# Kernel tuning notes

Measured on AMD Instinct MI355X. Metric: run time of the kernel, lower is better.

Reference implementation:

```python
import jax, jax.numpy as jnp
import numpy as np

N_USERS, N_ITEMS, N_GENRES = 31360, 6807, 18
TOTAL = N_USERS + N_ITEMS + N_GENRES          # 38185
OFFSET = TOTAL - N_GENRES                      # 38167
D = 16                                         # embedding_dim
B = 524288                                     # batch
MLP_DIMS = [64, 32, 16]
IN_DIM = 3 * D                                 # field_num * embedding_dim


def setup_inputs() -> dict:
    key = jax.random.key(0)
    ks = jax.random.split(key, 14)
    user = jax.random.randint(ks[0], (B, 1), 0, N_USERS)
    item = N_USERS + jax.random.randint(ks[1], (B, 1), 0, N_ITEMS)
    x_onehot = jnp.concatenate([user, item], axis=1)            # [B,2] global ids
    multi_hot = jax.random.randint(ks[2], (B, N_GENRES), 0, 2)  # [B,18] 0/1 mask
    s = 0.05
    emb_table = s * jax.random.normal(ks[3], (TOTAL, D), jnp.float32)
    fc_table = s * jax.random.normal(ks[4], (TOTAL, 1), jnp.float32)
    W1 = s * jax.random.normal(ks[5], (IN_DIM, MLP_DIMS[0]), jnp.float32)
    b1 = jnp.zeros((MLP_DIMS[0],), jnp.float32)
    W2 = s * jax.random.normal(ks[6], (MLP_DIMS[0], MLP_DIMS[1]), jnp.float32)
    b2 = jnp.zeros((MLP_DIMS[1],), jnp.float32)
    W3 = s * jax.random.normal(ks[7], (MLP_DIMS[1], MLP_DIMS[2]), jnp.float32)
    b3 = jnp.zeros((MLP_DIMS[2],), jnp.float32)
    W4 = s * jax.random.normal(ks[8], (MLP_DIMS[2], 1), jnp.float32)
    b4 = jnp.zeros((1,), jnp.float32)
    bias = jnp.zeros((1,), jnp.float32)
    return {"x_onehot": x_onehot, "multi_hot": multi_hot,
            "emb_table": emb_table, "fc_table": fc_table,
            "W1": W1, "b1": b1, "W2": W2, "b2": b2,
            "W3": W3, "b3": b3, "W4": W4, "b4": b4, "bias": bias}


def reference(x_onehot, multi_hot, emb_table, fc_table,
              W1, b1, W2, b2, W3, b3, W4, b4, bias):
    mh = multi_hot.astype(emb_table.dtype)                      # [B,18]
    # ragged multi-hot sum == mask @ genre slice of table (EmbeddingBag sum)
    embed_mh = mh @ emb_table[OFFSET:]                          # [B,D]
    embed_x = jnp.concatenate(
        [emb_table[x_onehot], embed_mh[:, None, :]], axis=1)    # [B,3,D]
    fc_mh = mh @ fc_table[OFFSET:]                              # [B,1]
    fc_x = jnp.concatenate(
        [fc_table[x_onehot], fc_mh[:, None, :]], axis=1)        # [B,3,1]
    # FM second-order term
    sum_e = embed_x.sum(axis=1)                                 # [B,D]
    fm_y = bias + fc_x.sum(axis=1) + 0.5 * jnp.sum(
        sum_e ** 2 - (embed_x ** 2).sum(axis=1), axis=1, keepdims=True)  # [B,1]
    # MLP (dropout inactive at inference)
    h = embed_x.reshape(embed_x.shape[0], -1)                   # [B,48]
    h = jax.nn.relu(h @ W1 + b1)
    h = jax.nn.relu(h @ W2 + b2)
    h = jax.nn.relu(h @ W3 + b3)
    mlp_y = h @ W4 + b4                                         # [B,1]
    return jax.nn.sigmoid(fm_y[:, 0] + mlp_y[:, 0])             # [B]
```

## Files before the change

### kernel.cpp

```cpp
#include <hip/hip_runtime.h>
#include <hip/hip_bf16.h>

namespace {

constexpr int kBatch  = 524288;
constexpr int kD      = 16;
constexpr int kOffset = 38167;
constexpr int kNG     = 18;

constexpr int W1B0   = 0;
constexpr int W2B0   = 8192;
constexpr int W3B0   = 12288;
constexpr int GB0    = 13312;
constexpr int WBYTES = 14336;

typedef __attribute__((ext_vector_type(8))) short short8;
typedef __attribute__((ext_vector_type(4))) float f32x4;

__device__ __forceinline__ unsigned short f2bf(float f) {
    return __builtin_bit_cast(unsigned short, __float2bfloat16(f));
}
__device__ __forceinline__ unsigned pk2(float a, float b) {
    return (unsigned)f2bf(a) | ((unsigned)f2bf(b) << 16);
}
__device__ __forceinline__ float bf2f(unsigned short s) {
    union { unsigned u; float f; } v; v.u = ((unsigned)s) << 16;
    return v.f;
}

__global__ void prep_weights(const float* __restrict__ emb,
                             const float* __restrict__ W1,
                             const float* __restrict__ W2,
                             const float* __restrict__ W3,
                             unsigned short* __restrict__ wimg)
{
    const int t = (int)threadIdx.x;
    for (int i = t; i < WBYTES / 2; i += 256) wimg[i] = 0;
    __syncthreads();
    for (int i = t; i < 48 * 64; i += 256) {
        int k = i >> 6, n = i & 63;
        int byte = W1B0 + n * 128 + ((k * 2) ^ ((n & 7) << 4));
        wimg[byte >> 1] = f2bf(W1[k * 64 + n]);
    }
    for (int i = t; i < 64 * 32; i += 256) {
        int k = i >> 5, n = i & 31;
        int byte = W2B0 + n * 128 + ((k * 2) ^ ((n & 7) << 4));
        wimg[byte >> 1] = f2bf(W2[k * 32 + n]);
    }
    for (int i = t; i < 32 * 16; i += 256) {
        int k = i >> 4, n = i & 15;
        int byte = W3B0 + n * 64 + ((k * 2) ^ ((n & 3) << 4));
        wimg[byte >> 1] = f2bf(W3[k * 16 + n]);
    }
    for (int i = t; i < 512; i += 256) {
        int c = i >> 5, r = i & 31, g = r >> 3, j = r & 7;
        int kg = 8 * g + j;
        wimg[(GB0 >> 1) + (4 * c + g) * 8 + j] =
            (kg < kNG) ? f2bf(emb[(size_t)(kOffset + kg) * kD + c]) : (unsigned short)0;
    }
}

__global__ __launch_bounds__(256, 3) void deepfm_fwd(
    const int*   __restrict__ x_onehot,
    const int*   __restrict__ multi_hot,
    const float* __restrict__ emb,
    const float* __restrict__ fc,
    const unsigned short* __restrict__ wimg,
    const float* __restrict__ b1,
    const float* __restrict__ b2,
    const float* __restrict__ b3,
    const float* __restrict__ W4,
    const float* __restrict__ b4,
    const float* __restrict__ bias,
    float*       __restrict__ out)
{
    __shared__ alignas(16) unsigned short s_w[WBYTES / 2];
    __shared__ alignas(16) unsigned short s_act[4 * 4096];

    const int t = (int)threadIdx.x;

    {
        const uint4* src = reinterpret_cast<const uint4*>(wimg);
        uint4*       dst = reinterpret_cast<uint4*>(s_w);
        #pragma unroll
        for (int q = 0; q < 4; ++q) {
            const int idx = t + 256 * q;
            if (idx < WBYTES / 16) dst[idx] = src[idx];
        }
    }

    const int i    = (int)blockIdx.x * 256 + t;
    const int lane = t & 63;
    const int w    = t >> 6;
    const int c    = lane & 15, g = lane >> 4;
    char* __restrict__ awc = (char*)(s_act + w * 4096);
    const char* __restrict__ swc = (const char*)s_w;

    const int l7 = lane & 7;
    const int sb = lane * 128;
    int rA[2];
    #pragma unroll
    for (int kt = 0; kt < 2; ++kt)
        rA[kt] = c * 128 + (((4 * kt + g) ^ (c & 7)) << 4);
    int wepi[4];
    #pragma unroll
    for (int nt = 0; nt < 4; ++nt)
        wepi[nt] = c * 128 + ((((2 * nt + (g >> 1)) ^ (c & 7))) << 4) + 8 * (g & 1);

    int2 mh[9];
    {
        const int2* mh2 = reinterpret_cast<const int2*>(multi_hot + (size_t)kNG * i);
        #pragma unroll
        for (int q = 0; q < 9; ++q) mh[q] = mh2[q];
    }
    const int2 ids = *reinterpret_cast<const int2*>(x_onehot + 2 * (size_t)i);

    float h[32];
    {
        const float4* eu = reinterpret_cast<const float4*>(emb + (size_t)ids.x * kD);
        #pragma unroll
        for (int q = 0; q < 4; ++q) {
            const float4 a = eu[q];
            h[4*q+0] = a.x; h[4*q+1] = a.y; h[4*q+2] = a.z; h[4*q+3] = a.w;
        }
        const float4* ei = reinterpret_cast<const float4*>(emb + (size_t)ids.y * kD);
        #pragma unroll
        for (int q = 0; q < 4; ++q) {
            const float4 a = ei[q];
            h[16+4*q+0] = a.x; h[16+4*q+1] = a.y; h[16+4*q+2] = a.z; h[16+4*q+3] = a.w;
        }
    }

    float4 b1q[4];
    #pragma unroll
    for (int nt = 0; nt < 4; ++nt)
        b1q[nt] = *reinterpret_cast<const float4*>(b1 + 16 * nt + 4 * g);
    float4 b2q[2];
    #pragma unroll
    for (int nt = 0; nt < 2; ++nt)
        b2q[nt] = *reinterpret_cast<const float4*>(b2 + 16 * nt + 4 * g);
    const float4 b3q = *reinterpret_cast<const float4*>(b3 + 4 * g);

    float lin = bias[0] + b4[0] + fc[ids.x] + fc[ids.y];
    #pragma unroll
    for (int q = 0; q < 9; ++q) {
        lin += mh[q].x ? fc[kOffset + 2 * q]     : 0.f;
        lin += mh[q].y ? fc[kOffset + 2 * q + 1] : 0.f;
    }

    {
        unsigned mw[9];
        #pragma unroll
        for (int q = 0; q < 9; ++q)
            mw[q] = (mh[q].x ? 0x3F80u : 0u) | (mh[q].y ? 0x3F800000u : 0u);
        uint4 v0; v0.x = mw[0]; v0.y = mw[1]; v0.z = mw[2]; v0.w = mw[3];
        uint4 v1; v1.x = mw[4]; v1.y = mw[5]; v1.z = mw[6]; v1.w = mw[7];
        uint4 v2; v2.x = mw[8]; v2.y = 0u;    v2.z = 0u;    v2.w = 0u;
        uint4 vz; vz.x = vz.y = vz.z = vz.w = 0u;
        *reinterpret_cast<uint4*>(awc + sb + (((0 ^ l7)) << 4)) = v0;
        *reinterpret_cast<uint4*>(awc + sb + (((1 ^ l7)) << 4)) = v1;
        *reinterpret_cast<uint4*>(awc + sb + (((2 ^ l7)) << 4)) = v2;
        *reinterpret_cast<uint4*>(awc + sb + (((3 ^ l7)) << 4)) = vz;
        *reinterpret_cast<uint4*>(awc + sb + (((6 ^ l7)) << 4)) = vz;
        *reinterpret_cast<uint4*>(awc + sb + (((7 ^ l7)) << 4)) = vz;
    }

    __syncthreads();

    const f32x4 z4 = {0.f, 0.f, 0.f, 0.f};

    {
        const short8 gfrag = *reinterpret_cast<const short8*>(s_w + (GB0 >> 1) + (4 * c + g) * 8);
        short8 bm[4];
        #pragma unroll
        for (int st = 0; st < 4; ++st)
            bm[st] = *reinterpret_cast<const short8*>(awc + rA[0] + 2048 * st);
        #pragma unroll
        for (int st = 0; st < 4; ++st) {
            const f32x4 accb = __builtin_amdgcn_mfma_f32_16x16x32_bf16(gfrag, bm[st], z4, 0, 0, 0);
            uint2 dv;
            dv.x = pk2(accb[0], accb[1]);
            dv.y = pk2(accb[2], accb[3]);
            *reinterpret_cast<uint2*>(awc + wepi[2] + 2048 * st) = dv;
        }
    }

    {
        #pragma unroll
        for (int q = 0; q < 4; ++q) {
            uint4 d;
            d.x = pk2(h[8*q+0], h[8*q+1]);
            d.y = pk2(h[8*q+2], h[8*q+3]);
            d.z = pk2(h[8*q+4], h[8*q+5]);
            d.w = pk2(h[8*q+6], h[8*q+7]);
            *reinterpret_cast<uint4*>(awc + sb + ((q ^ l7) << 4)) = d;
        }
    }

    float fm = 0.f;
    {
        const uint4 p0 = *reinterpret_cast<const uint4*>(awc + sb + ((4 ^ l7) << 4));
        const uint4 p1 = *reinterpret_cast<const uint4*>(awc + sb + ((5 ^ l7) << 4));
        const unsigned pp[8] = {p0.x, p0.y, p0.z, p0.w, p1.x, p1.y, p1.z, p1.w};
        float em[16];
        #pragma unroll
        for (int j = 0; j < 8; ++j) {
            em[2*j+0] = bf2f((unsigned short)(pp[j] & 0xFFFFu));
            em[2*j+1] = bf2f((unsigned short)(pp[j] >> 16));
        }
        #pragma unroll
        for (int d = 0; d < kD; ++d) fm = fmaf(h[d], h[16 + d], fm);
        #pragma unroll
        for (int d = 0; d < kD; ++d) fm = fmaf(h[d] + h[16 + d], em[d], fm);
    }

    f32x4 acc1[4][4];
    #pragma unroll
    for (int nt = 0; nt < 4; ++nt)
        #pragma unroll
        for (int st = 0; st < 4; ++st) acc1[nt][st] = z4;
    #pragma unroll
    for (int kt = 0; kt < 2; ++kt) {
        short8 aW[4], bA[4];
        #pragma unroll
        for (int nt = 0; nt < 4; ++nt)
            aW[nt] = *reinterpret_cast<const short8*>(swc + W1B0 + rA[kt] + 2048 * nt);
        #pragma unroll
        for (int st = 0; st < 4; ++st)
            bA[st] = *reinterpret_cast<const short8*>(awc + rA[kt] + 2048 * st);
        #pragma unroll
        for (int nt = 0; nt < 4; ++nt)
            #pragma unroll
            for (int st = 0; st < 4; ++st)
                acc1[nt][st] = __builtin_amdgcn_mfma_f32_16x16x32_bf16(aW[nt], bA[st], acc1[nt][st], 0, 0, 0);
    }
    #pragma unroll
    for (int nt = 0; nt < 4; ++nt)
        #pragma unroll
        for (int st = 0; st < 4; ++st) {
            const float v0 = fmaxf(acc1[nt][st][0] + b1q[nt].x, 0.f);
            const float v1 = fmaxf(acc1[nt][st][1] + b1q[nt].y, 0.f);
            const float v2 = fmaxf(acc1[nt][st][2] + b1q[nt].z, 0.f);
            const float v3 = fmaxf(acc1[nt][st][3] + b1q[nt].w, 0.f);
            uint2 dv; dv.x = pk2(v0, v1); dv.y = pk2(v2, v3);
            *reinterpret_cast<uint2*>(awc + wepi[nt] + 2048 * st) = dv;
        }

    f32x4 acc2[2][4];
    #pragma unroll
    for (int nt = 0; nt < 2; ++nt)
        #pragma unroll
        for (int st = 0; st < 4; ++st) acc2[nt][st] = z4;
    #pragma unroll
    for (int kt = 0; kt < 2; ++kt) {
        short8 aW[2], bA[4];
        #pragma unroll
        for (int nt = 0; nt < 2; ++nt)
            aW[nt] = *reinterpret_cast<const short8*>(swc + W2B0 + rA[kt] + 2048 * nt);
        #pragma unroll
        for (int st = 0; st < 4; ++st)
            bA[st] = *reinterpret_cast<const short8*>(awc + rA[kt] + 2048 * st);
        #pragma unroll
        for (int nt = 0; nt < 2; ++nt)
            #pragma unroll
            for (int st = 0; st < 4; ++st)
                acc2[nt][st] = __builtin_amdgcn_mfma_f32_16x16x32_bf16(aW[nt], bA[st], acc2[nt][st], 0, 0, 0);
    }
    #pragma unroll
    for (int nt = 0; nt < 2; ++nt)
        #pragma unroll
        for (int st = 0; st < 4; ++st) {
            const float v0 = fmaxf(acc2[nt][st][0] + b2q[nt].x, 0.f);
            const float v1 = fmaxf(acc2[nt][st][1] + b2q[nt].y, 0.f);
            const float v2 = fmaxf(acc2[nt][st][2] + b2q[nt].z, 0.f);
            const float v3 = fmaxf(acc2[nt][st][3] + b2q[nt].w, 0.f);
            uint2 dv; dv.x = pk2(v0, v1); dv.y = pk2(v2, v3);
            *reinterpret_cast<uint2*>(awc + wepi[nt] + 2048 * st) = dv;
        }

    {
        const short8 aW = *reinterpret_cast<const short8*>(
            swc + W3B0 + c * 64 + ((g ^ (c & 3)) << 4));
        short8 bA[4];
        #pragma unroll
        for (int st = 0; st < 4; ++st)
            bA[st] = *reinterpret_cast<const short8*>(awc + rA[0] + 2048 * st);
        #pragma unroll
        for (int st = 0; st < 4; ++st) {
            const f32x4 a3 = __builtin_amdgcn_mfma_f32_16x16x32_bf16(aW, bA[st], z4, 0, 0, 0);
            const float v0 = fmaxf(a3[0] + b3q.x, 0.f);
            const float v1 = fmaxf(a3[1] + b3q.y, 0.f);
            const float v2 = fmaxf(a3[2] + b3q.z, 0.f);
            const float v3 = fmaxf(a3[3] + b3q.w, 0.f);
            uint2 dv; dv.x = pk2(v0, v1); dv.y = pk2(v2, v3);
            *reinterpret_cast<uint2*>(awc + wepi[0] + 2048 * st) = dv;
        }
    }

    float mlp = 0.f;
    {
        const uint4 p0 = *reinterpret_cast<const uint4*>(awc + sb + ((0 ^ l7) << 4));
        const uint4 p1 = *reinterpret_cast<const uint4*>(awc + sb + ((1 ^ l7) << 4));
        const unsigned pp[8] = {p0.x, p0.y, p0.z, p0.w, p1.x, p1.y, p1.z, p1.w};
        #pragma unroll
        for (int j = 0; j < 8; ++j) {
            mlp = fmaf(bf2f((unsigned short)(pp[j] & 0xFFFFu)), W4[2*j],     mlp);
            mlp = fmaf(bf2f((unsigned short)(pp[j] >> 16)),     W4[2*j + 1], mlp);
        }
    }

    const float x = lin + fm + mlp;
    out[i] = 1.0f / (1.0f + __expf(-x));
}

}

extern "C" void kernel_launch(void* const* d_in, const int* in_sizes, int n_in,
                              void* d_out, int out_size, void* d_ws, size_t ws_size,
                              hipStream_t stream) {
    (void)in_sizes; (void)n_in; (void)ws_size; (void)out_size;
    const int*   x_onehot  = (const int*)  d_in[0];
    const int*   multi_hot = (const int*)  d_in[1];
    const float* emb       = (const float*)d_in[2];
    const float* fc        = (const float*)d_in[3];
    const float* W1        = (const float*)d_in[4];
    const float* b1        = (const float*)d_in[5];
    const float* W2        = (const float*)d_in[6];
    const float* b2        = (const float*)d_in[7];
    const float* W3        = (const float*)d_in[8];
    const float* b3        = (const float*)d_in[9];
    const float* W4        = (const float*)d_in[10];
    const float* b4        = (const float*)d_in[11];
    const float* biasp     = (const float*)d_in[12];
    float* out = (float*)d_out;
    unsigned short* wimg = (unsigned short*)d_ws;

    hipLaunchKernelGGL(prep_weights, dim3(1), dim3(256), 0, stream,
                       emb, W1, W2, W3, wimg);
    hipLaunchKernelGGL(deepfm_fwd, dim3(kBatch / 256), dim3(256), 0, stream,
                       x_onehot, multi_hot, emb, fc, wimg,
                       b1, b2, b3, W4, b4, biasp, out);
}
```

Baseline: 42.44 us.

## Fuse final MLP layer via wave shuffles and restructure LDS staging order

Computes the last layer's W4 dot product directly from the layer-3 MFMA accumulators, reducing across lanes with xor-shuffles instead of writing bf16 results to LDS and reading them back. The multi-hot mask is now staged into a different LDS slot so the embedding writes can happen before the single barrier, and part of the FM term is computed before the sync. Layer-1 and layer-2 MFMA loops are reordered per sample tile, with the epilogue folded in, to shorten accumulator live ranges. This adds shuffle and select work and depends on the lane-to-sample mapping being correct.

```diff
diff --git a/kernel.cpp b/kernel.cpp
--- a/kernel.cpp
+++ b/kernel.cpp
@@ -140,6 +140,7 @@
     for (int nt = 0; nt < 2; ++nt)
         b2q[nt] = *reinterpret_cast<const float4*>(b2 + 16 * nt + 4 * g);
     const float4 b3q = *reinterpret_cast<const float4*>(b3 + 4 * g);
+    const float4 w4q = *reinterpret_cast<const float4*>(W4 + 4 * g);
 
     float lin = bias[0] + b4[0] + fc[ids.x] + fc[ids.y];
     #pragma unroll
@@ -157,32 +158,10 @@
         uint4 v1; v1.x = mw[4]; v1.y = mw[5]; v1.z = mw[6]; v1.w = mw[7];
         uint4 v2; v2.x = mw[8]; v2.y = 0u;    v2.z = 0u;    v2.w = 0u;
         uint4 vz; vz.x = vz.y = vz.z = vz.w = 0u;
-        *reinterpret_cast<uint4*>(awc + sb + (((0 ^ l7)) << 4)) = v0;
-        *reinterpret_cast<uint4*>(awc + sb + (((1 ^ l7)) << 4)) = v1;
-        *reinterpret_cast<uint4*>(awc + sb + (((2 ^ l7)) << 4)) = v2;
-        *reinterpret_cast<uint4*>(awc + sb + (((3 ^ l7)) << 4)) = vz;
-        *reinterpret_cast<uint4*>(awc + sb + (((6 ^ l7)) << 4)) = vz;
-        *reinterpret_cast<uint4*>(awc + sb + (((7 ^ l7)) << 4)) = vz;
-    }
-
-    __syncthreads();
-
-    const f32x4 z4 = {0.f, 0.f, 0.f, 0.f};
-
-    {
-        const short8 gfrag = *reinterpret_cast<const short8*>(s_w + (GB0 >> 1) + (4 * c + g) * 8);
-        short8 bm[4];
-        #pragma unroll
-        for (int st = 0; st < 4; ++st)
-            bm[st] = *reinterpret_cast<const short8*>(awc + rA[0] + 2048 * st);
-        #pragma unroll
-        for (int st = 0; st < 4; ++st) {
-            const f32x4 accb = __builtin_amdgcn_mfma_f32_16x16x32_bf16(gfrag, bm[st], z4, 0, 0, 0);
-            uint2 dv;
-            dv.x = pk2(accb[0], accb[1]);
-            dv.y = pk2(accb[2], accb[3]);
-            *reinterpret_cast<uint2*>(awc + wepi[2] + 2048 * st) = dv;
-        }
+        *reinterpret_cast<uint4*>(awc + sb + ((4 ^ l7) << 4)) = v0;
+        *reinterpret_cast<uint4*>(awc + sb + ((5 ^ l7) << 4)) = v1;
+        *reinterpret_cast<uint4*>(awc + sb + ((6 ^ l7) << 4)) = v2;
+        *reinterpret_cast<uint4*>(awc + sb + ((7 ^ l7) << 4)) = vz;
     }
 
     {
@@ -198,86 +177,114 @@
     }
 
     float fm = 0.f;
+    #pragma unroll
+    for (int d = 0; d < kD; ++d) fm = fmaf(h[d], h[16 + d], fm);
+
+    __syncthreads();
+
+    const f32x4 z4 = {0.f, 0.f, 0.f, 0.f};
+
+    {
+        const short8 gfrag = *reinterpret_cast<const short8*>(s_w + (GB0 >> 1) + (4 * c + g) * 8);
+        short8 bm[4];
+        #pragma unroll
+        for (int st = 0; st < 4; ++st)
+            bm[st] = *reinterpret_cast<const short8*>(awc + rA[1] + 2048 * st);
+        #pragma unroll
+        for (int st = 0; st < 4; ++st) {
+            const f32x4 accb = __builtin_amdgcn_mfma_f32_16x16x32_bf16(gfrag, bm[st], z4, 0, 0, 0);
+            uint2 dv;
+            dv.x = pk2(accb[0], accb[1]);
+            dv.y = pk2(accb[2], accb[3]);
+            *reinterpret_cast<uint2*>(awc + wepi[2] + 2048 * st) = dv;
+        }
+        uint4 vz; vz.x = vz.y = vz.z = vz.w = 0u;
+        *reinterpret_cast<uint4*>(awc + sb + ((6 ^ l7) << 4)) = vz;
+        *reinterpret_cast<uint4*>(awc + sb + ((7 ^ l7) << 4)) = vz;
+    }
+
     {
         const uint4 p0 = *reinterpret_cast<const uint4*>(awc + sb + ((4 ^ l7) << 4));
         const uint4 p1 = *reinterpret_cast<const uint4*>(awc + sb + ((5 ^ l7) << 4));
         const unsigned pp[8] = {p0.x, p0.y, p0.z, p0.w, p1.x, p1.y, p1.z, p1.w};
-        float em[16];
         #pragma unroll
         for (int j = 0; j < 8; ++j) {
-            em[2*j+0] = bf2f((unsigned short)(pp[j] & 0xFFFFu));
-            em[2*j+1] = bf2f((unsigned short)(pp[j] >> 16));
-        }
-        #pragma unroll
-        for (int d = 0; d < kD; ++d) fm = fmaf(h[d], h[16 + d], fm);
-        #pragma unroll
-        for (int d = 0; d < kD; ++d) fm = fmaf(h[d] + h[16 + d], em[d], fm);
-    }
-
-    f32x4 acc1[4][4];
-    #pragma unroll
-    for (int nt = 0; nt < 4; ++nt)
-        #pragma unroll
-        for (int st = 0; st < 4; ++st) acc1[nt][st] = z4;
-    #pragma unroll
-    for (int kt = 0; kt < 2; ++kt) {
-        short8 aW[4], bA[4];
+            const float e0 = bf2f((unsigned short)(pp[j] & 0xFFFFu));
+            const float e1 = bf2f((unsigned short)(pp[j] >> 16));
+            fm = fmaf(h[2*j]   + h[16 + 2*j],   e0, fm);
+            fm = fmaf(h[2*j+1] + h[16 + 2*j+1], e1, fm);
+        }
+    }
+
+    {
+        short8 aW[4][2], bA[4][2];
         #pragma unroll
         for (int nt = 0; nt < 4; ++nt)
-            aW[nt] = *reinterpret_cast<const short8*>(swc + W1B0 + rA[kt] + 2048 * nt);
+            #pragma unroll
+            for (int kt = 0; kt < 2; ++kt)
+                aW[nt][kt] = *reinterpret_cast<const short8*>(swc + W1B0 + rA[kt] + 2048 * nt);
         #pragma unroll
         for (int st = 0; st < 4; ++st)
-            bA[st] = *reinterpret_cast<const short8*>(awc + rA[kt] + 2048 * st);
-        #pragma unroll
-        for (int nt = 0; nt < 4; ++nt)
-            #pragma unroll
-            for (int st = 0; st < 4; ++st)
-                acc1[nt][st] = __builtin_amdgcn_mfma_f32_16x16x32_bf16(aW[nt], bA[st], acc1[nt][st], 0, 0, 0);
-    }
-    #pragma unroll
-    for (int nt = 0; nt < 4; ++nt)
+            #pragma unroll
+            for (int kt = 0; kt < 2; ++kt)
+                bA[st][kt] = *reinterpret_cast<const short8*>(awc + rA[kt] + 2048 * st);
         #pragma unroll
         for (int st = 0; st < 4; ++st) {
-            const float v0 = fmaxf(acc1[nt][st][0] + b1q[nt].x, 0.f);
-            const float v1 = fmaxf(acc1[nt][st][1] + b1q[nt].y, 0.f);
-            const float v2 = fmaxf(acc1[nt][st][2] + b1q[nt].z, 0.f);
-            const float v3 = fmaxf(acc1[nt][st][3] + b1q[nt].w, 0.f);
-            uint2 dv; dv.x = pk2(v0, v1); dv.y = pk2(v2, v3);
-            *reinterpret_cast<uint2*>(awc + wepi[nt] + 2048 * st) = dv;
-        }
-
-    f32x4 acc2[2][4];
-    #pragma unroll
-    for (int nt = 0; nt < 2; ++nt)
-        #pragma unroll
-        for (int st = 0; st < 4; ++st) acc2[nt][st] = z4;
-    #pragma unroll
-    for (int kt = 0; kt < 2; ++kt) {
-        short8 aW[2], bA[4];
+            f32x4 acc[4];
+            #pragma unroll
+            for (int nt = 0; nt < 4; ++nt) acc[nt] = z4;
+            #pragma unroll
+            for (int kt = 0; kt < 2; ++kt)
+                #pragma unroll
+                for (int nt = 0; nt < 4; ++nt)
+                    acc[nt] = __builtin_amdgcn_mfma_f32_16x16x32_bf16(aW[nt][kt], bA[st][kt], acc[nt], 0, 0, 0);
+            #pragma unroll
+            for (int nt = 0; nt < 4; ++nt) {
+                const float v0 = fmaxf(acc[nt][0] + b1q[nt].x, 0.f);
+                const float v1 = fmaxf(acc[nt][1] + b1q[nt].y, 0.f);
+                const float v2 = fmaxf(acc[nt][2] + b1q[nt].z, 0.f);
+                const float v3 = fmaxf(acc[nt][3] + b1q[nt].w, 0.f);
+                uint2 dv; dv.x = pk2(v0, v1); dv.y = pk2(v2, v3);
+                *reinterpret_cast<uint2*>(awc + wepi[nt] + 2048 * st) = dv;
+            }
+        }
+    }
+
+    {
+        short8 aW[2][2], bA[4][2];
         #pragma unroll
         for (int nt = 0; nt < 2; ++nt)
-            aW[nt] = *reinterpret_cast<const short8*>(swc + W2B0 + rA[kt] + 2048 * nt);
+            #pragma unroll
+            for (int kt = 0; kt < 2; ++kt)
+                aW[nt][kt] = *reinterpret_cast<const short8*>(swc + W2B0 + rA[kt] + 2048 * nt);
         #pragma unroll
         for (int st = 0; st < 4; ++st)
-            bA[st] = *reinterpret_cast<const short8*>(awc + rA[kt] + 2048 * st);
-        #pragma unroll
-        for (int nt = 0; nt < 2; ++nt)
-            #pragma unroll
-            for (int st = 0; st < 4; ++st)
-                acc2[nt][st] = __builtin_amdgcn_mfma_f32_16x16x32_bf16(aW[nt], bA[st], acc2[nt][st], 0, 0, 0);
-    }
-    #pragma unroll
-    for (int nt = 0; nt < 2; ++nt)
+            #pragma unroll
+            for (int kt = 0; kt < 2; ++kt)
+                bA[st][kt] = *reinterpret_cast<const short8*>(awc + rA[kt] + 2048 * st);
         #pragma unroll
         for (int st = 0; st < 4; ++st) {
-            const float v0 = fmaxf(acc2[nt][st][0] + b2q[nt].x, 0.f);
-            const float v1 = fmaxf(acc2[nt][st][1] + b2q[nt].y, 0.f);
-            const float v2 = fmaxf(acc2[nt][st][2] + b2q[nt].z, 0.f);
-            const float v3 = fmaxf(acc2[nt][st][3] + b2q[nt].w, 0.f);
-            uint2 dv; dv.x = pk2(v0, v1); dv.y = pk2(v2, v3);
-            *reinterpret_cast<uint2*>(awc + wepi[nt] + 2048 * st) = dv;
-        }
-
+            f32x4 acc[2];
+            #pragma unroll
+            for (int nt = 0; nt < 2; ++nt) acc[nt] = z4;
+            #pragma unroll
+            for (int kt = 0; kt < 2; ++kt)
+                #pragma unroll
+                for (int nt = 0; nt < 2; ++nt)
+                    acc[nt] = __builtin_amdgcn_mfma_f32_16x16x32_bf16(aW[nt][kt], bA[st][kt], acc[nt], 0, 0, 0);
+            #pragma unroll
+            for (int nt = 0; nt < 2; ++nt) {
+                const float v0 = fmaxf(acc[nt][0] + b2q[nt].x, 0.f);
+                const float v1 = fmaxf(acc[nt][1] + b2q[nt].y, 0.f);
+                const float v2 = fmaxf(acc[nt][2] + b2q[nt].z, 0.f);
+                const float v3 = fmaxf(acc[nt][3] + b2q[nt].w, 0.f);
+                uint2 dv; dv.x = pk2(v0, v1); dv.y = pk2(v2, v3);
+                *reinterpret_cast<uint2*>(awc + wepi[nt] + 2048 * st) = dv;
+            }
+        }
+    }
+
+    float tot[4];
     {
         const short8 aW = *reinterpret_cast<const short8*>(
             swc + W3B0 + c * 64 + ((g ^ (c & 3)) << 4));
@@ -288,26 +295,19 @@
         #pragma unroll
         for (int st = 0; st < 4; ++st) {
             const f32x4 a3 = __builtin_amdgcn_mfma_f32_16x16x32_bf16(aW, bA[st], z4, 0, 0, 0);
-            const float v0 = fmaxf(a3[0] + b3q.x, 0.f);
-            const float v1 = fmaxf(a3[1] + b3q.y, 0.f);
-            const float v2 = fmaxf(a3[2] + b3q.z, 0.f);
-            const float v3 = fmaxf(a3[3] + b3q.w, 0.f);
-            uint2 dv; dv.x = pk2(v0, v1); dv.y = pk2(v2, v3);
-            *reinterpret_cast<uint2*>(awc + wepi[0] + 2048 * st) = dv;
-        }
-    }
-
-    float mlp = 0.f;
-    {
-        const uint4 p0 = *reinterpret_cast<const uint4*>(awc + sb + ((0 ^ l7) << 4));
-        const uint4 p1 = *reinterpret_cast<const uint4*>(awc + sb + ((1 ^ l7) << 4));
-        const unsigned pp[8] = {p0.x, p0.y, p0.z, p0.w, p1.x, p1.y, p1.z, p1.w};
-        #pragma unroll
-        for (int j = 0; j < 8; ++j) {
-            mlp = fmaf(bf2f((unsigned short)(pp[j] & 0xFFFFu)), W4[2*j],     mlp);
-            mlp = fmaf(bf2f((unsigned short)(pp[j] >> 16)),     W4[2*j + 1], mlp);
-        }
-    }
+            float p = 0.f;
+            p = fmaf(fmaxf(a3[0] + b3q.x, 0.f), w4q.x, p);
+            p = fmaf(fmaxf(a3[1] + b3q.y, 0.f), w4q.y, p);
+            p = fmaf(fmaxf(a3[2] + b3q.z, 0.f), w4q.z, p);
+            p = fmaf(fmaxf(a3[3] + b3q.w, 0.f), w4q.w, p);
+            p += __shfl_xor(p, 16, 64);
+            p += __shfl_xor(p, 32, 64);
+            tot[st] = p;
+        }
+    }
+    const float m01 = (g & 1) ? tot[1] : tot[0];
+    const float m23 = (g & 1) ? tot[3] : tot[2];
+    const float mlp = (g & 2) ? m23 : m01;
 
     const float x = lin + fm + mlp;
     out[i] = 1.0f / (1.0f + __expf(-x));
```

After: 38.78 us. 8.6% less time.
